# Kernel tuning notes

Measured on AMD Instinct MI355X. Metric: run time of the kernel, lower is better.

## Reference

```python
import jax, jax.numpy as jnp
import numpy as np

N = 12288
IN_F = 256
OUT_F = 128
SLOPE = 0.2
MASK_VAL = -9e16


def setup_inputs() -> dict:
    key = jax.random.key(0)
    k1, k2, k3, k4 = jax.random.split(key, 4)
    h = jax.random.normal(k1, (N, IN_F), dtype=jnp.float32)
    adj_matrix = jax.random.randint(k2, (N, N), 0, 2, dtype=jnp.int32)
    W = jax.random.normal(k3, (IN_F, OUT_F), dtype=jnp.float32) * (1.0 / np.sqrt(IN_F))
    a = jax.random.normal(k4, (2 * OUT_F, 1), dtype=jnp.float32) * (1.0 / np.sqrt(2 * OUT_F))
    return {"h": h, "adj_matrix": adj_matrix, "W": W, "a": a}


def reference(h, adj_matrix, W, a):
    # eval mode: F.dropout is identity
    h_t = h @ W                              # [N, OUT_F]
    src = h_t @ a[:OUT_F]                    # [N, 1]
    tgt = h_t @ a[OUT_F:]                    # [N, 1]
    e = src + tgt.T                          # [N, N] additive scores
    e = jnp.where(e >= 0, e, SLOPE * e)      # leaky relu
    e = jnp.where(adj_matrix > 0, e, MASK_VAL)
    attention = jax.nn.softmax(e, axis=-1)   # [N, N]
    h_prime = attention @ h_t                # [N, OUT_F]
    return (h_prime, attention)
```

## Files before the change

### kernel.cpp

```cpp
#include <hip/hip_runtime.h>
#include <hip/hip_bf16.h>
#include <stdint.h>

#define NN 12288
#define INF_ 256
#define OUTF 128
#define SLOPE 0.2f
#define JSPLIT 8
#define CPB (NN/128/JSPLIT)

typedef __bf16 bf16x8 __attribute__((ext_vector_type(8)));
typedef float f32x16 __attribute__((ext_vector_type(16)));
typedef float f32x4 __attribute__((ext_vector_type(4)));
typedef uint32_t u32x4 __attribute__((ext_vector_type(4)));

union BFU { u32x4 u; bf16x8 b; };

__device__ __forceinline__ float bflo(uint32_t u){ return __uint_as_float(u << 16); }
__device__ __forceinline__ float bfhi(uint32_t u){ return __uint_as_float(u & 0xffff0000u); }
__device__ __forceinline__ uint32_t f2bf(float f){
    union { __bf16 b; uint16_t s; } u; u.b = (__bf16)f; return (uint32_t)u.s;
}
__device__ __forceinline__ void unpack8(u32x4 u, float* f){
    f[0]=bflo(u.x); f[1]=bfhi(u.x); f[2]=bflo(u.y); f[3]=bfhi(u.y);
    f[4]=bflo(u.z); f[5]=bfhi(u.z); f[6]=bflo(u.w); f[7]=bfhi(u.w);
}

__global__ __launch_bounds__(256) void k0_detect(const uint32_t* __restrict__ hw,
                                                 uint32_t* __restrict__ flag)
{
    __shared__ int cnt[4];
    int t = threadIdx.x;
    uint32_t w = hw[t];
    uint32_t e = (w >> 7) & 0xffu;
    int s = (e >= 110u && e <= 140u) ? 1 : 0;
    #pragma unroll
    for (int mm=1;mm<64;mm<<=1) s += __shfl_xor(s,mm,64);
    if ((t&63)==0) cnt[t>>6]=s;
    __syncthreads();
    if (t==0) flag[0] = ((cnt[0]+cnt[1]+cnt[2]+cnt[3]) < 128) ? 1u : 0u;
}

__global__ __launch_bounds__(256) void k1_ht(
    const void* __restrict__ h, const void* __restrict__ Wp,
    const void* __restrict__ a, const uint32_t* __restrict__ flagp,
    uint16_t* __restrict__ packed, float* __restrict__ src, float* __restrict__ tgt)
{
    __shared__ __align__(16) uint16_t tile[16*128];
    int t = threadIdx.x;
    int rloc = t >> 4;
    int row = blockIdx.x*16 + rloc;
    int f0 = (t & 15) * 8;
    bool f32in = flagp[0] != 0u;

    float acc[8];
    #pragma unroll
    for (int c=0;c<8;c++) acc[c]=0.f;
    float a1f[8], a2f[8];

    if (f32in){
        const float* hrow = (const float*)h + (size_t)row*INF_;
        const float* Wf   = (const float*)Wp;
        for (int k=0;k<INF_;k+=8){
            float hv[8];
            *(f32x4*)&hv[0] = *(const f32x4*)(hrow + k);
            *(f32x4*)&hv[4] = *(const f32x4*)(hrow + k + 4);
            #pragma unroll
            for (int i=0;i<8;i++){
                const float* w0 = Wf + (size_t)(k+i)*OUTF + f0;
                float wf[8];
                *(f32x4*)&wf[0] = *(const f32x4*)w0;
                *(f32x4*)&wf[4] = *(const f32x4*)(w0+4);
                #pragma unroll
                for (int c=0;c<8;c++) acc[c] = fmaf(hv[i], wf[c], acc[c]);
            }
        }
        const float* af = (const float*)a;
        *(f32x4*)&a1f[0] = *(const f32x4*)(af + f0);
        *(f32x4*)&a1f[4] = *(const f32x4*)(af + f0 + 4);
        *(f32x4*)&a2f[0] = *(const f32x4*)(af + OUTF + f0);
        *(f32x4*)&a2f[4] = *(const f32x4*)(af + OUTF + f0 + 4);
    } else {
        const uint16_t* hrow = (const uint16_t*)h + (size_t)row*INF_;
        const uint16_t* W16  = (const uint16_t*)Wp;
        for (int k=0;k<INF_;k+=8){
            u32x4 hu = *(const u32x4*)(hrow + k);
            float hv[8]; unpack8(hu,hv);
            #pragma unroll
            for (int i=0;i<8;i++){
                u32x4 wu = *(const u32x4*)(W16 + (size_t)(k+i)*OUTF + f0);
                float wf[8]; unpack8(wu,wf);
                #pragma unroll
                for (int c=0;c<8;c++) acc[c] = fmaf(hv[i], wf[c], acc[c]);
            }
        }
        const uint16_t* a16 = (const uint16_t*)a;
        u32x4 a1u = *(const u32x4*)(a16 + f0);
        u32x4 a2u = *(const u32x4*)(a16 + OUTF + f0);
        unpack8(a1u,a1f); unpack8(a2u,a2f);
    }

    float p1=0.f, p2=0.f;
    #pragma unroll
    for (int c=0;c<8;c++){ p1 = fmaf(acc[c],a1f[c],p1); p2 = fmaf(acc[c],a2f[c],p2); }
    #pragma unroll
    for (int mm=1;mm<16;mm<<=1){ p1 += __shfl_xor(p1,mm,64); p2 += __shfl_xor(p2,mm,64); }
    if ((t&15)==0){ src[row]=p1; tgt[row]=p2; }

    uint32_t q0 = f2bf(acc[0]) | (f2bf(acc[1])<<16);
    uint32_t q1 = f2bf(acc[2]) | (f2bf(acc[3])<<16);
    uint32_t q2 = f2bf(acc[4]) | (f2bf(acc[5])<<16);
    uint32_t q3 = f2bf(acc[6]) | (f2bf(acc[7])<<16);
    u32x4 pk = {q0,q1,q2,q3};
    *(u32x4*)&tile[rloc*128 + f0] = pk;
    __syncthreads();
    int n = t >> 1, kb = (t & 1) * 8;
    uint32_t g0 = (uint32_t)tile[(kb+0)*128+n] | ((uint32_t)tile[(kb+1)*128+n]<<16);
    uint32_t g1 = (uint32_t)tile[(kb+2)*128+n] | ((uint32_t)tile[(kb+3)*128+n]<<16);
    uint32_t g2 = (uint32_t)tile[(kb+4)*128+n] | ((uint32_t)tile[(kb+5)*128+n]<<16);
    uint32_t g3 = (uint32_t)tile[(kb+6)*128+n] | ((uint32_t)tile[(kb+7)*128+n]<<16);
    u32x4 ov = {g0,g1,g2,g3};
    *(u32x4*)(packed + (size_t)blockIdx.x*2048 + t*8) = ov;
}

__global__ __launch_bounds__(256) void k1b_max(const float* __restrict__ tgt,
                                               float* __restrict__ maxtgt)
{
    __shared__ float red[4];
    int t = threadIdx.x;
    float m = -3.4e38f;
    for (int j=t; j<NN; j+=256) m = fmaxf(m, tgt[j]);
    #pragma unroll
    for (int mm=1;mm<64;mm<<=1) m = fmaxf(m, __shfl_xor(m,mm,64));
    if ((t&63)==0) red[t>>6]=m;
    __syncthreads();
    if (t==0) maxtgt[0] = fmaxf(fmaxf(red[0],red[1]), fmaxf(red[2],red[3]));
}

__global__ __launch_bounds__(256) void k1c_zero(float* __restrict__ hp)
{
    int i = blockIdx.x*256 + threadIdx.x;
    f32x4 z = {0.f,0.f,0.f,0.f};
    *(f32x4*)(hp + (size_t)i*4) = z;
}

__global__ __launch_bounds__(256) void k2_mask(
    const int* __restrict__ adj, const float* __restrict__ src,
    const float* __restrict__ maxtgt, const float* __restrict__ tgt,
    uint32_t* __restrict__ bm, float* __restrict__ Mrow, float* __restrict__ Srow)
{
    __shared__ float ls[4];
    int row = blockIdx.x, t = threadIdx.x;
    float sr = src[row];
    float e0 = sr + maxtgt[0];
    float M  = fmaxf(e0, SLOPE*e0);
    const u32x4* arow = (const u32x4*)(adj + (size_t)row*NN);
    uint32_t* bmrow = bm + (size_t)row*384;
    float sum = 0.f;
    #pragma unroll
    for (int jb=0;jb<12;jb++){
        int j0 = jb*1024 + t*4;
        u32x4 a4 = __builtin_nontemporal_load(arow + jb*256 + t);
        float4 t4 = *(const float4*)(tgt + j0);
        uint32_t nib = (a4.x!=0u) | ((a4.y!=0u)<<1) | ((a4.z!=0u)<<2) | ((a4.w!=0u)<<3);
        float ev, lv, pv;
        ev = sr + t4.x; lv = fmaxf(ev, SLOPE*ev); pv = __expf(lv - M); sum += (nib&1u)     ? pv : 0.f;
        ev = sr + t4.y; lv = fmaxf(ev, SLOPE*ev); pv = __expf(lv - M); sum += ((nib>>1)&1u)? pv : 0.f;
        ev = sr + t4.z; lv = fmaxf(ev, SLOPE*ev); pv = __expf(lv - M); sum += ((nib>>2)&1u)? pv : 0.f;
        ev = sr + t4.w; lv = fmaxf(ev, SLOPE*ev); pv = __expf(lv - M); sum += ((nib>>3)&1u)? pv : 0.f;
        uint32_t wv = nib << ((t&7)*4);
        wv |= __shfl_xor(wv,1,64); wv |= __shfl_xor(wv,2,64); wv |= __shfl_xor(wv,4,64);
        if ((t&7)==0) __builtin_nontemporal_store(wv, bmrow + jb*32 + (t>>3));
    }
    #pragma unroll
    for (int mm=1;mm<64;mm<<=1) sum += __shfl_xor(sum,mm,64);
    if ((t&63)==0) ls[t>>6]=sum;
    __syncthreads();
    if (t==0){ Srow[row] = ls[0]+ls[1]+ls[2]+ls[3]; Mrow[row] = M; }
}

__global__ __launch_bounds__(256) void k3_pv(
    const uint32_t* __restrict__ bm, const float* __restrict__ tgt,
    const float* __restrict__ src, const float* __restrict__ Mrow,
    const float* __restrict__ Srow, const uint16_t* __restrict__ packed,
    const uint32_t* __restrict__ flagp, float* __restrict__ hp,
    void* __restrict__ out)
{
    __shared__ __align__(16) uint16_t P[32*136];
    int t = threadIdx.x;
    int lane = t & 63, wv = t >> 6;
    int r0 = blockIdx.x * 32;
    int rr0 = t >> 4;
    int jg  = t & 15; int jl0 = jg*8;
    int n0 = wv*32;
    int m = lane & 31, kq = lane >> 5;
    bool f32out = flagp[0] != 0u;

    uint16_t* hprime16 = (uint16_t*)out;
    uint16_t* attn16   = hprime16 + (size_t)NN*OUTF;
    float*    hprimef  = (float*)out;
    float*    attnf    = hprimef + (size_t)NN*OUTF;

    float s0 = src[r0+rr0],      s1 = src[r0+rr0+16];
    float M0 = Mrow[r0+rr0],     M1 = Mrow[r0+rr0+16];
    float S0 = Srow[r0+rr0],     S1 = Srow[r0+rr0+16];
    float inv0 = S0>0.f ? 1.f/S0 : 0.f;  float fb0 = S0>0.f ? 0.f : 1.f/NN;
    float inv1 = S1>0.f ? 1.f/S1 : 0.f;  float fb1 = S1>0.f ? 0.f : 1.f/NN;

    f32x16 acc;
    #pragma unroll
    for (int i=0;i<16;i++) acc[i]=0.f;

    int cs = blockIdx.y * CPB;
    for (int c=cs; c<cs+CPB; c++){
        int jbase = c*128;
        float tg[8];
        *(f32x4*)&tg[0] = *(const f32x4*)(tgt + jbase + jl0);
        *(f32x4*)&tg[4] = *(const f32x4*)(tgt + jbase + jl0 + 4);
        #pragma unroll
        for (int hh=0;hh<2;hh++){
            int rr = rr0 + hh*16;
            uint32_t word = bm[(size_t)(r0+rr)*384 + (c<<2) + (jg>>2)];
            uint32_t byt  = (word >> ((jg&3)*8)) & 0xffu;
            float sv = hh? s1:s0, Mv = hh? M1:M0, iv = hh? inv1:inv0, fv = hh? fb1:fb0;
            uint32_t pk[4];
            float pf[8];
            #pragma unroll
            for (int i=0;i<4;i++){
                float ea = sv + tg[2*i],   eb = sv + tg[2*i+1];
                float la = fmaxf(ea, SLOPE*ea), lb = fmaxf(eb, SLOPE*eb);
                float pa = ((byt>>(2*i))&1u)   ? __expf(la-Mv)*iv : fv;
                float pb = ((byt>>(2*i+1))&1u) ? __expf(lb-Mv)*iv : fv;
                pk[i] = f2bf(pa) | (f2bf(pb)<<16);
                pf[2*i] = pa; pf[2*i+1] = pb;
            }
            u32x4 pv4 = {pk[0],pk[1],pk[2],pk[3]};
            if (f32out){
                f32x4 fa = {pf[0],pf[1],pf[2],pf[3]};
                f32x4 fb = {pf[4],pf[5],pf[6],pf[7]};
                float* dst = attnf + (size_t)(r0+rr)*NN + jbase + jl0;
                __builtin_nontemporal_store(fa, (f32x4*)dst);
                __builtin_nontemporal_store(fb, (f32x4*)(dst+4));
            } else {
                __builtin_nontemporal_store(pv4,
                    (u32x4*)(attn16 + (size_t)(r0+rr)*NN + jbase + jl0));
            }
            *(u32x4*)&P[rr*136 + jl0] = pv4;
        }
        __syncthreads();
        #pragma unroll
        for (int kt=0;kt<8;kt++){
            BFU A; A.u = *(const u32x4*)&P[m*136 + (kt<<4) + (kq<<3)];
            BFU B; B.u = *(const u32x4*)(packed +
                        (((size_t)(c*8+kt))<<11) + ((size_t)(n0+m)<<4) + (kq<<3));
            acc = __builtin_amdgcn_mfma_f32_32x32x16_bf16(A.b, B.b, acc, 0, 0, 0);
        }
        __syncthreads();
    }
    #pragma unroll
    for (int r=0;r<16;r++){
        int orow = (r&3) + 8*(r>>2) + 4*kq;
        atomicAdd(&hp[(size_t)(r0+orow)*OUTF + n0 + m], acc[r]);
    }
}

__global__ __launch_bounds__(256) void k4_fin(const float* __restrict__ hp,
    const uint32_t* __restrict__ flagp, void* __restrict__ out)
{
    int t = blockIdx.x*256 + threadIdx.x;
    size_t base = (size_t)t*8;
    bool f32out = flagp[0] != 0u;
    f32x4 v0 = *(const f32x4*)(hp + base);
    f32x4 v1 = *(const f32x4*)(hp + base + 4);
    if (f32out){
        float* o = (float*)out;
        *(f32x4*)(o + base)     = v0;
        *(f32x4*)(o + base + 4) = v1;
    } else {
        uint32_t q0 = f2bf(v0.x) | (f2bf(v0.y)<<16);
        uint32_t q1 = f2bf(v0.z) | (f2bf(v0.w)<<16);
        uint32_t q2 = f2bf(v1.x) | (f2bf(v1.y)<<16);
        uint32_t q3 = f2bf(v1.z) | (f2bf(v1.w)<<16);
        u32x4 pk = {q0,q1,q2,q3};
        *(u32x4*)((uint16_t*)out + base) = pk;
    }
}

extern "C" void kernel_launch(void* const* d_in, const int* in_sizes, int n_in,
                              void* d_out, int out_size, void* d_ws, size_t ws_size,
                              hipStream_t stream)
{
    const void* h  = d_in[0];
    const int*  adj= (const int*)d_in[1];
    const void* W  = d_in[2];
    const void* a  = d_in[3];

    char* ws = (char*)d_ws;
    uint16_t* packed = (uint16_t*)ws;
    float* src    = (float*)(ws + 3145728);
    float* tgt    = (float*)(ws + 3194880);
    float* Mrow   = (float*)(ws + 3244032);
    float* Srow   = (float*)(ws + 3293184);
    float* maxtgt = (float*)(ws + 3342336);
    uint32_t* flag= (uint32_t*)(ws + 3342400);
    uint32_t* bm  = (uint32_t*)(ws + 3342464);
    float* hp     = (float*)(ws + 22216832);

    k0_detect<<<dim3(1),    dim3(256), 0, stream>>>((const uint32_t*)h, flag);
    k1_ht    <<<dim3(NN/16),dim3(256), 0, stream>>>(h, W, a, flag, packed, src, tgt);
    k1b_max  <<<dim3(1),    dim3(256), 0, stream>>>(tgt, maxtgt);
    k1c_zero <<<dim3(NN*OUTF/1024), dim3(256), 0, stream>>>(hp);
    k2_mask  <<<dim3(NN),   dim3(256), 0, stream>>>(adj, src, maxtgt, tgt, bm, Mrow, Srow);
    k3_pv    <<<dim3(NN/32, JSPLIT), dim3(256), 0, stream>>>(bm, tgt, src, Mrow, Srow,
                                                             packed, flag, hp, d_out);
    k4_fin   <<<dim3(NN*OUTF/2048), dim3(256), 0, stream>>>(hp, flag, d_out);
}
```

Baseline: 1.134 ms.

## Fold detect/max/zero kernels into neighbors and replace atomics with split partial buffers

Removes the separate detect, max-reduction and zeroing kernels by inlining input-format detection into each kernel and computing the max target score with an ordered-int atomicMax inside k1. The PV kernel now writes per-split partial results to separate buffers instead of issuing atomicAdd, and the finalize kernel sums the partials. The column split is halved. This cuts launch overhead and atomic traffic, in exchange for more workspace and extra reads in the finalize step.

```diff
diff --git a/kernel.cpp b/kernel.cpp
--- a/kernel.cpp
+++ b/kernel.cpp
@@ -6,7 +6,7 @@
 #define INF_ 256
 #define OUTF 128
 #define SLOPE 0.2f
-#define JSPLIT 8
+#define JSPLIT 4
 #define CPB (NN/128/JSPLIT)
 
 typedef __bf16 bf16x8 __attribute__((ext_vector_type(8)));
@@ -26,32 +26,41 @@
     f[4]=bflo(u.z); f[5]=bfhi(u.z); f[6]=bflo(u.w); f[7]=bfhi(u.w);
 }
 
-__global__ __launch_bounds__(256) void k0_detect(const uint32_t* __restrict__ hw,
-                                                 uint32_t* __restrict__ flag)
-{
-    __shared__ int cnt[4];
-    int t = threadIdx.x;
-    uint32_t w = hw[t];
+__device__ __forceinline__ uint32_t fenc(float f){
+    uint32_t b = __float_as_uint(f);
+    return b ^ ((b & 0x80000000u) ? 0xFFFFFFFFu : 0x80000000u);
+}
+__device__ __forceinline__ float fdec(uint32_t e){
+    uint32_t b = e ^ ((e & 0x80000000u) ? 0x80000000u : 0xFFFFFFFFu);
+    return __uint_as_float(b);
+}
+
+__device__ __forceinline__ bool detect_f32(const uint32_t* hw, int t, int* cnt){
+    uint32_t w = hw[t & 255];
     uint32_t e = (w >> 7) & 0xffu;
     int s = (e >= 110u && e <= 140u) ? 1 : 0;
     #pragma unroll
     for (int mm=1;mm<64;mm<<=1) s += __shfl_xor(s,mm,64);
     if ((t&63)==0) cnt[t>>6]=s;
     __syncthreads();
-    if (t==0) flag[0] = ((cnt[0]+cnt[1]+cnt[2]+cnt[3]) < 128) ? 1u : 0u;
+    return (cnt[0]+cnt[1]+cnt[2]+cnt[3]) < 128;
 }
 
 __global__ __launch_bounds__(256) void k1_ht(
     const void* __restrict__ h, const void* __restrict__ Wp,
-    const void* __restrict__ a, const uint32_t* __restrict__ flagp,
-    uint16_t* __restrict__ packed, float* __restrict__ src, float* __restrict__ tgt)
+    const void* __restrict__ a,
+    uint16_t* __restrict__ packed, float* __restrict__ src, float* __restrict__ tgt,
+    uint32_t* __restrict__ maxtgt)
 {
     __shared__ __align__(16) uint16_t tile[16*128];
+    __shared__ int cnt[4];
+    __shared__ float wmax[4];
     int t = threadIdx.x;
+    bool f32in = detect_f32((const uint32_t*)h, t, cnt);
+
     int rloc = t >> 4;
     int row = blockIdx.x*16 + rloc;
     int f0 = (t & 15) * 8;
-    bool f32in = flagp[0] != 0u;
 
     float acc[8];
     #pragma unroll
@@ -107,6 +116,11 @@
     for (int mm=1;mm<16;mm<<=1){ p1 += __shfl_xor(p1,mm,64); p2 += __shfl_xor(p2,mm,64); }
     if ((t&15)==0){ src[row]=p1; tgt[row]=p2; }
 
+    float bmx = p2;
+    #pragma unroll
+    for (int mm=16;mm<64;mm<<=1) bmx = fmaxf(bmx, __shfl_xor(bmx,mm,64));
+    if ((t&63)==0) wmax[t>>6] = bmx;
+
     uint32_t q0 = f2bf(acc[0]) | (f2bf(acc[1])<<16);
     uint32_t q1 = f2bf(acc[2]) | (f2bf(acc[3])<<16);
     uint32_t q2 = f2bf(acc[4]) | (f2bf(acc[5])<<16);
@@ -114,6 +128,10 @@
     u32x4 pk = {q0,q1,q2,q3};
     *(u32x4*)&tile[rloc*128 + f0] = pk;
     __syncthreads();
+    if (t==0){
+        float m4 = fmaxf(fmaxf(wmax[0],wmax[1]), fmaxf(wmax[2],wmax[3]));
+        atomicMax(maxtgt, fenc(m4));
+    }
     int n = t >> 1, kb = (t & 1) * 8;
     uint32_t g0 = (uint32_t)tile[(kb+0)*128+n] | ((uint32_t)tile[(kb+1)*128+n]<<16);
     uint32_t g1 = (uint32_t)tile[(kb+2)*128+n] | ((uint32_t)tile[(kb+3)*128+n]<<16);
@@ -123,36 +141,15 @@
     *(u32x4*)(packed + (size_t)blockIdx.x*2048 + t*8) = ov;
 }
 
-__global__ __launch_bounds__(256) void k1b_max(const float* __restrict__ tgt,
-                                               float* __restrict__ maxtgt)
-{
-    __shared__ float red[4];
-    int t = threadIdx.x;
-    float m = -3.4e38f;
-    for (int j=t; j<NN; j+=256) m = fmaxf(m, tgt[j]);
-    #pragma unroll
-    for (int mm=1;mm<64;mm<<=1) m = fmaxf(m, __shfl_xor(m,mm,64));
-    if ((t&63)==0) red[t>>6]=m;
-    __syncthreads();
-    if (t==0) maxtgt[0] = fmaxf(fmaxf(red[0],red[1]), fmaxf(red[2],red[3]));
-}
-
-__global__ __launch_bounds__(256) void k1c_zero(float* __restrict__ hp)
-{
-    int i = blockIdx.x*256 + threadIdx.x;
-    f32x4 z = {0.f,0.f,0.f,0.f};
-    *(f32x4*)(hp + (size_t)i*4) = z;
-}
-
 __global__ __launch_bounds__(256) void k2_mask(
     const int* __restrict__ adj, const float* __restrict__ src,
-    const float* __restrict__ maxtgt, const float* __restrict__ tgt,
+    const uint32_t* __restrict__ maxtgt, const float* __restrict__ tgt,
     uint32_t* __restrict__ bm, float* __restrict__ Mrow, float* __restrict__ Srow)
 {
     __shared__ float ls[4];
     int row = blockIdx.x, t = threadIdx.x;
     float sr = src[row];
-    float e0 = sr + maxtgt[0];
+    float e0 = sr + fdec(maxtgt[0]);
     float M  = fmaxf(e0, SLOPE*e0);
     const u32x4* arow = (const u32x4*)(adj + (size_t)row*NN);
     uint32_t* bmrow = bm + (size_t)row*384;
@@ -183,23 +180,23 @@
     const uint32_t* __restrict__ bm, const float* __restrict__ tgt,
     const float* __restrict__ src, const float* __restrict__ Mrow,
     const float* __restrict__ Srow, const uint16_t* __restrict__ packed,
-    const uint32_t* __restrict__ flagp, float* __restrict__ hp,
+    const void* __restrict__ h, float* __restrict__ hp,
     void* __restrict__ out)
 {
     __shared__ __align__(16) uint16_t P[32*136];
+    __shared__ int cnt[4];
     int t = threadIdx.x;
+    bool f32out = detect_f32((const uint32_t*)h, t, cnt);
+
     int lane = t & 63, wv = t >> 6;
     int r0 = blockIdx.x * 32;
     int rr0 = t >> 4;
     int jg  = t & 15; int jl0 = jg*8;
     int n0 = wv*32;
     int m = lane & 31, kq = lane >> 5;
-    bool f32out = flagp[0] != 0u;
-
-    uint16_t* hprime16 = (uint16_t*)out;
-    uint16_t* attn16   = hprime16 + (size_t)NN*OUTF;
-    float*    hprimef  = (float*)out;
-    float*    attnf    = hprimef + (size_t)NN*OUTF;
+
+    uint16_t* attn16 = (uint16_t*)out + (size_t)NN*OUTF;
+    float*    attnf  = (float*)out + (size_t)NN*OUTF;
 
     float s0 = src[r0+rr0],      s1 = src[r0+rr0+16];
     float M0 = Mrow[r0+rr0],     M1 = Mrow[r0+rr0+16];
@@ -257,21 +254,29 @@
         }
         __syncthreads();
     }
+    float* hpp = hp + (size_t)blockIdx.y * ((size_t)NN*OUTF);
     #pragma unroll
     for (int r=0;r<16;r++){
         int orow = (r&3) + 8*(r>>2) + 4*kq;
-        atomicAdd(&hp[(size_t)(r0+orow)*OUTF + n0 + m], acc[r]);
+        hpp[(size_t)(r0+orow)*OUTF + n0 + m] = acc[r];
     }
 }
 
 __global__ __launch_bounds__(256) void k4_fin(const float* __restrict__ hp,
-    const uint32_t* __restrict__ flagp, void* __restrict__ out)
-{
-    int t = blockIdx.x*256 + threadIdx.x;
-    size_t base = (size_t)t*8;
-    bool f32out = flagp[0] != 0u;
-    f32x4 v0 = *(const f32x4*)(hp + base);
-    f32x4 v1 = *(const f32x4*)(hp + base + 4);
+    const void* __restrict__ h, void* __restrict__ out)
+{
+    __shared__ int cnt[4];
+    int t = threadIdx.x;
+    bool f32out = detect_f32((const uint32_t*)h, t, cnt);
+    size_t base = ((size_t)blockIdx.x*256 + t)*8;
+    f32x4 v0 = {0.f,0.f,0.f,0.f}, v1 = {0.f,0.f,0.f,0.f};
+    #pragma unroll
+    for (int y=0;y<JSPLIT;y++){
+        const float* p = hp + (size_t)y*((size_t)NN*OUTF) + base;
+        f32x4 a0 = *(const f32x4*)p;
+        f32x4 a1 = *(const f32x4*)(p+4);
+        v0 += a0; v1 += a1;
+    }
     if (f32out){
         float* o = (float*)out;
         *(f32x4*)(o + base)     = v0;
@@ -301,17 +306,14 @@
     float* tgt    = (float*)(ws + 3194880);
     float* Mrow   = (float*)(ws + 3244032);
     float* Srow   = (float*)(ws + 3293184);
-    float* maxtgt = (float*)(ws + 3342336);
-    uint32_t* flag= (uint32_t*)(ws + 3342400);
+    uint32_t* maxtgt = (uint32_t*)(ws + 3342336);
     uint32_t* bm  = (uint32_t*)(ws + 3342464);
     float* hp     = (float*)(ws + 22216832);
 
-    k0_detect<<<dim3(1),    dim3(256), 0, stream>>>((const uint32_t*)h, flag);
-    k1_ht    <<<dim3(NN/16),dim3(256), 0, stream>>>(h, W, a, flag, packed, src, tgt);
-    k1b_max  <<<dim3(1),    dim3(256), 0, stream>>>(tgt, maxtgt);
-    k1c_zero <<<dim3(NN*OUTF/1024), dim3(256), 0, stream>>>(hp);
-    k2_mask  <<<dim3(NN),   dim3(256), 0, stream>>>(adj, src, maxtgt, tgt, bm, Mrow, Srow);
-    k3_pv    <<<dim3(NN/32, JSPLIT), dim3(256), 0, stream>>>(bm, tgt, src, Mrow, Srow,
-                                                             packed, flag, hp, d_out);
-    k4_fin   <<<dim3(NN*OUTF/2048), dim3(256), 0, stream>>>(hp, flag, d_out);
-}
+    hipMemsetAsync(maxtgt, 0, 4, stream);
+    k1_ht  <<<dim3(NN/16),dim3(256), 0, stream>>>(h, W, a, packed, src, tgt, maxtgt);
+    k2_mask<<<dim3(NN),   dim3(256), 0, stream>>>(adj, src, maxtgt, tgt, bm, Mrow, Srow);
+    k3_pv  <<<dim3(NN/32, JSPLIT), dim3(256), 0, stream>>>(bm, tgt, src, Mrow, Srow,
+                                                           packed, h, hp, d_out);
+    k4_fin <<<dim3(NN*OUTF/2048), dim3(256), 0, stream>>>(hp, h, d_out);
+}
```

After: 1.133 ms. No clear change (-0.1%).
